# Performance work log

Measured on AMD Instinct MI355X. Metric: run time of the kernel, lower is better.

The kernel has to match this reference:

```python
import jax, jax.numpy as jnp
import numpy as np

B, CIN, H, W = 16, 128, 56, 56
COUT, KH, KW = 256, 3, 3
STRIDE = (1, 1)
PAD = ((1, 1), (1, 1))


def setup_inputs() -> dict:
    key = jax.random.key(0)
    k1, k2, k3 = jax.random.split(key, 3)
    x = jax.random.normal(k1, (B, CIN, H, W), dtype=jnp.float32)
    weight = jax.random.normal(k2, (COUT, CIN, KH, KW), dtype=jnp.float32) * 0.05
    bias = jax.random.normal(k3, (COUT,), dtype=jnp.float32)
    return {"x": x, "weight": weight, "bias": bias}


def reference(x, weight, bias):
    # Conv2d with zero padding, stride 1 -- identical math to the torch
    # unfold+expand+multiply+triple-sum path.
    dn = jax.lax.conv_dimension_numbers(x.shape, weight.shape, ("NCHW", "OIHW", "NCHW"))
    out = jax.lax.conv_general_dilated(x, weight, STRIDE, PAD, dimension_numbers=dn)
    out = out + bias[None, :, None, None]

    # Sparsity of the elementwise product patches * weight.
    # count_nonzero(x_patch * w) over all (b,hw,ww,co,ci,kh,kw) factorizes as
    # sum over windows of conv(1[x!=0], 1[w!=0]) -- same count without
    # materializing the [B,Hw,Ww,Co,Ci,kh,kw] tensor the torch code builds.
    co, ci, kh, kw = weight.shape
    hw, ww = out.shape[2], out.shape[3]
    num_elements = x.shape[0] * hw * ww * co * ci * kh * kw
    nz_map = jax.lax.conv_general_dilated(
        (x != 0).astype(jnp.float32),
        (weight != 0).astype(jnp.float32),
        STRIDE, PAD, dimension_numbers=dn)
    num_nonzero = jnp.sum(nz_map)
    layer_sparsity = (jnp.float32(num_elements) - num_nonzero) / jnp.float32(num_elements)
    return out, layer_sparsity
```

## Files before the change

### kernel.cpp

```cpp
#include <hip/hip_runtime.h>
#include <hip/hip_bf16.h>

typedef __attribute__((ext_vector_type(8))) short bf16x8;
typedef __attribute__((ext_vector_type(8))) unsigned short ushort8;
typedef __attribute__((ext_vector_type(4))) unsigned short ushort4v;
typedef __attribute__((ext_vector_type(4))) float f32x4;
typedef __attribute__((ext_vector_type(4))) unsigned int uint4v;

#define CIN_  128
#define BATCH 16
#define SP_   3136
#define CO_   256
#define NTOT  50176

#define XP_BYTES   13778944
#define WT_BYTES   589824
#define WS_NEEDED  14447104

__device__ __forceinline__ unsigned short f2bf(float f) {
    unsigned int u = __float_as_uint(f);
    u = (u + 0x7fffu + ((u >> 16) & 1u)) >> 16;
    return (unsigned short)u;
}

__device__ __forceinline__ void gl_lds16(const unsigned short* g, unsigned short* l) {
    __builtin_amdgcn_global_load_lds(
        (const __attribute__((address_space(1))) unsigned int*)g,
        (__attribute__((address_space(3))) unsigned int*)l, 16, 0, 0);
}

__global__ __launch_bounds__(256) void k_aux(
    const float* __restrict__ x, const float* __restrict__ w,
    unsigned short* __restrict__ Wt, unsigned short* __restrict__ xp,
    float* __restrict__ Wcnt, float* __restrict__ part)
{
    __shared__ float T[64][65];
    __shared__ float red9[4][9];
    const int blk = blockIdx.x;
    const int tid = threadIdx.x;

    if (blk < 288) {
        int base = (blk * 256 + tid) * 4;
        float4 v = *(const float4*)(w + base);
        #pragma unroll
        for (int j = 0; j < 4; ++j) {
            int e = base + j;
            int co = e / 1152;
            int r  = e - co * 1152;
            int ci = r / 9;
            int koff = r - ci * 9;
            Wt[(koff * 256 + co) * 128 + ci] = f2bf(((const float*)&v)[j]);
        }
    } else if (blk < 576) {
        int lane = tid & 63;
        int j = (blk - 288) * 4 + (tid >> 6);
        float c = 0.f;
        for (int co = lane; co < 256; co += 64)
            c += (w[(size_t)co * 1152 + j] != 0.0f) ? 1.f : 0.f;
        #pragma unroll
        for (int s = 32; s > 0; s >>= 1) c += __shfl_down(c, s, 64);
        if (lane == 0) Wcnt[j] = c;
    } else if (blk < 2624) {
        int bc = blk - 576;
        int ci = bc & 127;
        int b  = bc >> 7;
        const float* xpk = x + (size_t)bc * SP_;
        float cnt[9];
        #pragma unroll
        for (int k = 0; k < 9; ++k) cnt[k] = 0.f;
        for (int e = tid; e < SP_; e += 256) {
            float v = xpk[e];
            if (v != 0.f) {
                int h = e / 56, w_ = e - h * 56;
                float r0 = (h <= 54) ? 1.f : 0.f;
                float r2 = (h >= 1) ? 1.f : 0.f;
                float c0 = (w_ <= 54) ? 1.f : 0.f;
                float c2 = (w_ >= 1) ? 1.f : 0.f;
                cnt[0] += r0 * c0; cnt[1] += r0; cnt[2] += r0 * c2;
                cnt[3] += c0;      cnt[4] += 1.f; cnt[5] += c2;
                cnt[6] += r2 * c0; cnt[7] += r2; cnt[8] += r2 * c2;
            }
        }
        #pragma unroll
        for (int k = 0; k < 9; ++k) {
            #pragma unroll
            for (int s = 32; s > 0; s >>= 1) cnt[k] += __shfl_down(cnt[k], s, 64);
        }
        if ((tid & 63) == 0) {
            #pragma unroll
            for (int k = 0; k < 9; ++k) red9[tid >> 6][k] = cnt[k];
        }
        __syncthreads();
        if (tid < 9) {
            float s = red9[0][tid] + red9[1][tid] + red9[2][tid] + red9[3][tid];
            part[(ci * 9 + tid) * 16 + b] = s;
        }
    } else if (blk < 4192) {
        int i = blk - 2624;
        int sp0 = (i % 49) * 64;
        int rest = i / 49;
        int ci0 = (rest & 1) * 64;
        int b = rest >> 1;
        const float* xb = x + ((size_t)(b * 128 + ci0)) * SP_ + sp0;
        #pragma unroll
        for (int r = 0; r < 16; ++r) {
            const int ci_l = (tid >> 6) * 16 + r;
            const int sp_l = tid & 63;
            T[sp_l][ci_l] = xb[(size_t)ci_l * SP_ + sp_l];
        }
        __syncthreads();
        #pragma unroll
        for (int r = 0; r < 4; ++r) {
            const int sp_l = (tid >> 4) * 4 + r;
            const int cc   = (tid & 15) * 4;
            const int sp = sp0 + sp_l;
            const int oh = sp / 56, ow = sp - oh * 56;
            ushort4v v;
            #pragma unroll
            for (int j = 0; j < 4; ++j) v[j] = f2bf(T[sp_l][cc + j]);
            *(ushort4v*)&xp[(((size_t)b * 58 + oh + 1) * 58 + (ow + 1)) * 128 + ci0 + cc] = v;
        }
    } else {
        int b = blk - 4192;
        if (tid < 228) {
            int oh, ow;
            if (tid < 58)       { oh = 0;            ow = tid; }
            else if (tid < 116) { oh = 57;           ow = tid - 58; }
            else if (tid < 172) { oh = tid - 116 + 1; ow = 0; }
            else                { oh = tid - 172 + 1; ow = 57; }
            unsigned short* p = xp + (((size_t)b * 58 + oh) * 58 + ow) * 128;
            ushort8 z = {};
            #pragma unroll
            for (int j = 0; j < 16; ++j) *(ushort8*)(p + j * 8) = z;
        }
    }
}

__global__ void k_spars(const float* __restrict__ Wcnt, const float* __restrict__ part,
                        float* __restrict__ out_scalar) {
    __shared__ double red[256];
    int t = threadIdx.x;
    double s = 0.0;
    for (int j = t; j < 1152; j += 256) {
        const float4* p4 = (const float4*)(part + (size_t)j * 16);
        float4 a = p4[0], b = p4[1], c = p4[2], d = p4[3];
        float xs = (a.x + a.y + a.z + a.w) + (b.x + b.y + b.z + b.w)
                 + (c.x + c.y + c.z + c.w) + (d.x + d.y + d.z + d.w);
        s += (double)Wcnt[j] * (double)xs;
    }
    red[t] = s; __syncthreads();
    for (int k = 128; k > 0; k >>= 1) {
        if (t < k) red[t] += red[t + k];
        __syncthreads();
    }
    if (t == 0) {
        const double ne = 14797504512.0;
        out_scalar[0] = (float)((ne - red[0]) / ne);
    }
}

__global__ __launch_bounds__(512, 2) void k_conv8(
    const unsigned short* __restrict__ xp, const unsigned short* __restrict__ Wt,
    const float* __restrict__ bias, float* __restrict__ out)
{
    __shared__ __attribute__((aligned(16))) unsigned short Albs[4 * 8192];
    __shared__ __attribute__((aligned(16))) unsigned short Blbs[4 * 8192];

    const int tid  = threadIdx.x;
    const int lane = tid & 63;
    const int l15  = lane & 15;
    const int w    = tid >> 6;
    const int wm   = w >> 2;
    const int wn   = w & 3;
    const int n0   = blockIdx.x * 256;

    int xoffA[2], woffB[2];
    #pragma unroll
    for (int j = 0; j < 2; ++j) {
        int g   = j * 512 + tid;
        int row = g >> 2;
        int c   = (g & 3) ^ ((row >> 1) & 3);
        int n   = n0 + row;
        int b   = n / SP_;
        int sp  = n - b * SP_;
        int oh  = sp / 56, ow = sp - oh * 56;
        xoffA[j] = ((b * 58 + oh + 1) * 58 + (ow + 1)) * 128 + c * 8;
        woffB[j] = row * 128 + c * 8;
    }

    auto stageA = [&](int slotoff, int xsh) {
        #pragma unroll
        for (int j = 0; j < 2; ++j)
            gl_lds16(xp + xsh + xoffA[j], &Albs[slotoff + (j * 512 + tid) * 8]);
    };
    auto stageB = [&](int slotoff, int wsh) {
        #pragma unroll
        for (int j = 0; j < 2; ++j)
            gl_lds16(Wt + wsh + woffB[j], &Blbs[slotoff + (j * 512 + tid) * 8]);
    };

    f32x4 acc[8][4] = {};
    const int cl = lane >> 4;

#define LDA_(SLOT, R) \
    (*(const bf16x8*)&Albs[(SLOT) * 8192 + ((R) + l15) * 32 + \
        ((cl ^ ((((R) + l15) >> 1) & 3)) * 8)])
#define LDB_(SLOT, R) \
    (*(const bf16x8*)&Blbs[(SLOT) * 8192 + ((R) + l15) * 32 + \
        ((cl ^ ((((R) + l15) >> 1) & 3)) * 8)])

    {
        const int xsh0 = (-59) * 128;
        stageA(0, xsh0);          stageB(0, 0);
        stageA(8192, xsh0 + 32);  stageB(8192, 32);
        asm volatile("s_waitcnt vmcnt(4)" ::: "memory");
        __builtin_amdgcn_s_barrier();
    }

    #pragma unroll 1
    for (int koff = 0; koff < 9; ++koff) {
        #pragma unroll
        for (int q = 0; q < 4; ++q) {
            const int p = koff * 4 + q;
            const int slot = q;

            bf16x8 b_[4], a_[8];
            #pragma unroll
            for (int nn = 0; nn < 4; ++nn) b_[nn] = LDB_(slot, wn * 64 + nn * 16);
            #pragma unroll
            for (int m = 0; m < 8; ++m)    a_[m] = LDA_(slot, wm * 128 + m * 16);

            if (p + 2 <= 35) {
                const int p2  = p + 2;
                const int ko2 = p2 >> 2;
                const int q2  = p2 & 3;
                const int kd2 = ko2 / 3;
                const int xsh = ((kd2 - 1) * 58 + (ko2 - kd2 * 3 - 1)) * 128 + q2 * 32;
                const int wsh = ko2 * 32768 + q2 * 32;
                stageA(q2 * 8192, xsh);
                stageB(q2 * 8192, wsh);
                asm volatile("s_waitcnt vmcnt(4)" ::: "memory");
            } else {
                asm volatile("s_waitcnt vmcnt(0)" ::: "memory");
            }
            __builtin_amdgcn_s_barrier();

            __builtin_amdgcn_s_setprio(1);
            #pragma unroll
            for (int m = 0; m < 8; ++m)
                #pragma unroll
                for (int nn = 0; nn < 4; ++nn)
                    acc[m][nn] = __builtin_amdgcn_mfma_f32_16x16x32_bf16(
                        a_[m], b_[nn], acc[m][nn], 0, 0, 0);
            __builtin_amdgcn_s_setprio(0);
        }
    }

#undef LDA_
#undef LDB_

    #pragma unroll
    for (int m = 0; m < 8; ++m) {
        int n  = n0 + wm * 128 + m * 16 + (lane >> 4) * 4;
        int b  = n / SP_;
        int sp = n - b * SP_;
        #pragma unroll
        for (int nn = 0; nn < 4; ++nn) {
            int co = wn * 64 + nn * 16 + l15;
            f32x4 v = acc[m][nn] + bias[co];
            *(f32x4*)&out[((size_t)(b * CO_ + co)) * SP_ + sp] = v;
        }
    }
}

__global__ void k_wt(const float* __restrict__ w, unsigned short* __restrict__ Wt) {
    int e = blockIdx.x * 256 + threadIdx.x;
    float v = w[e];
    int co = e / 1152;
    int r  = e - co * 1152;
    int ci = r / 9;
    int koff = r - ci * 9;
    Wt[(koff * 256 + co) * 128 + ci] = f2bf(v);
}

__global__ void k_wcnt(const float* __restrict__ w, float* __restrict__ Wcnt) {
    int j = blockIdx.x;
    int lane = threadIdx.x;
    float c = 0.f;
    for (int co = lane; co < 256; co += 64)
        c += (w[(size_t)co * 1152 + j] != 0.0f) ? 1.f : 0.f;
    #pragma unroll
    for (int s = 32; s > 0; s >>= 1) c += __shfl_down(c, s, 64);
    if (lane == 0) Wcnt[j] = c;
}

__global__ void k_xcnt(const float* __restrict__ x, float* __restrict__ Xcnt) {
    int blk = blockIdx.x;
    int ci = blk & 127;
    const float* xpk = x + (size_t)blk * SP_;
    int tid = threadIdx.x;
    float cnt[9];
    #pragma unroll
    for (int k = 0; k < 9; ++k) cnt[k] = 0.f;
    for (int e = tid; e < SP_; e += 256) {
        float v = xpk[e];
        if (v != 0.f) {
            int h = e / 56, w_ = e - h * 56;
            float r0 = (h <= 54) ? 1.f : 0.f;
            float r2 = (h >= 1) ? 1.f : 0.f;
            float c0 = (w_ <= 54) ? 1.f : 0.f;
            float c2 = (w_ >= 1) ? 1.f : 0.f;
            cnt[0] += r0 * c0; cnt[1] += r0; cnt[2] += r0 * c2;
            cnt[3] += c0;      cnt[4] += 1.f; cnt[5] += c2;
            cnt[6] += r2 * c0; cnt[7] += r2; cnt[8] += r2 * c2;
        }
    }
    #pragma unroll
    for (int k = 0; k < 9; ++k) {
        #pragma unroll
        for (int s = 32; s > 0; s >>= 1) cnt[k] += __shfl_down(cnt[k], s, 64);
    }
    if ((tid & 63) == 0) {
        #pragma unroll
        for (int k = 0; k < 9; ++k)
            atomicAdd(&Xcnt[ci * 9 + k], cnt[k]);
    }
}

__global__ void k_spars_f(const float* __restrict__ Wcnt, const float* __restrict__ Xcnt,
                          float* __restrict__ out_scalar) {
    __shared__ double red[256];
    int t = threadIdx.x;
    double s = 0.0;
    for (int j = t; j < 1152; j += 256)
        s += (double)Wcnt[j] * (double)Xcnt[j];
    red[t] = s; __syncthreads();
    for (int k = 128; k > 0; k >>= 1) {
        if (t < k) red[t] += red[t + k];
        __syncthreads();
    }
    if (t == 0) {
        const double ne = 14797504512.0;
        out_scalar[0] = (float)((ne - red[0]) / ne);
    }
}

__global__ __launch_bounds__(256) void k_conv(
    const float* __restrict__ x, const unsigned short* __restrict__ Wt,
    const float* __restrict__ bias, float* __restrict__ out)
{
    __shared__ __attribute__((aligned(16))) unsigned short AldsF[64][40];
    __shared__ __attribute__((aligned(16))) unsigned short BldsF[64][40];

    const int tid  = threadIdx.x;
    const int lane = tid & 63;
    const int wid  = tid >> 6;
    const int wm   = wid >> 1, wn = wid & 1;

    const int n0  = blockIdx.x * 64;
    const int b   = blockIdx.x / 49;
    const int sp0 = n0 - b * SP_;
    const int co0 = blockIdx.y * 64;

    const int a_co = tid >> 2;
    const int a_ci = (tid & 3) * 8;
    const int b_n  = tid & 63;
    const int b_k0 = (tid >> 6) * 8;

    const int sp = sp0 + b_n;
    const int oh = sp / 56, ow = sp - oh * 56;

    f32x4 acc[2][2] = {};
    const float* xb_base = x + (size_t)b * CIN_ * SP_;

    for (int koff = 0; koff < 9; ++koff) {
        const int dh = koff / 3 - 1, dw = koff - (koff / 3) * 3 - 1;
        const int ih = oh + dh, iw = ow + dw;
        const bool valid = ((unsigned)ih < 56u) && ((unsigned)iw < 56u);
        const float* xb = xb_base + sp + dh * 56 + dw;
        const unsigned short* wp = Wt + ((size_t)(koff * 256 + co0 + a_co)) * 128 + a_ci;

        for (int ci0 = 0; ci0 < 128; ci0 += 32) {
            uint4v av = *(const uint4v*)(wp + ci0);
            *(uint4v*)&AldsF[a_co][a_ci] = av;
            ushort8 bv;
            #pragma unroll
            for (int j = 0; j < 8; ++j) {
                int ci = ci0 + b_k0 + j;
                float v = 0.f;
                if (valid) v = xb[(size_t)ci * SP_];
                bv[j] = f2bf(v);
            }
            *(ushort8*)&BldsF[b_n][b_k0] = bv;
            __syncthreads();

            const int row = lane & 15;
            const int kq  = (lane >> 4) * 8;
            bf16x8 a0 = *(const bf16x8*)&AldsF[wm * 32 + row][kq];
            bf16x8 a1 = *(const bf16x8*)&AldsF[wm * 32 + 16 + row][kq];
            bf16x8 bb0 = *(const bf16x8*)&BldsF[wn * 32 + row][kq];
            bf16x8 bb1 = *(const bf16x8*)&BldsF[wn * 32 + 16 + row][kq];
            acc[0][0] = __builtin_amdgcn_mfma_f32_16x16x32_bf16(a0, bb0, acc[0][0], 0, 0, 0);
            acc[0][1] = __builtin_amdgcn_mfma_f32_16x16x32_bf16(a0, bb1, acc[0][1], 0, 0, 0);
            acc[1][0] = __builtin_amdgcn_mfma_f32_16x16x32_bf16(a1, bb0, acc[1][0], 0, 0, 0);
            acc[1][1] = __builtin_amdgcn_mfma_f32_16x16x32_bf16(a1, bb1, acc[1][1], 0, 0, 0);
            __syncthreads();
        }
    }

    const int col = lane & 15;
    const int rb  = (lane >> 4) * 4;
    #pragma unroll
    for (int f = 0; f < 2; ++f) {
        #pragma unroll
        for (int g = 0; g < 2; ++g) {
            int spc = sp0 + wn * 32 + g * 16 + col;
            #pragma unroll
            for (int r = 0; r < 4; ++r) {
                int co = co0 + wm * 32 + f * 16 + rb + r;
                out[((size_t)(b * CO_ + co)) * SP_ + spc] = acc[f][g][r] + bias[co];
            }
        }
    }
}

extern "C" void kernel_launch(void* const* d_in, const int* in_sizes, int n_in,
                              void* d_out, int out_size, void* d_ws, size_t ws_size,
                              hipStream_t stream) {
    const float* x    = (const float*)d_in[0];
    const float* w    = (const float*)d_in[1];
    const float* bias = (const float*)d_in[2];
    float* out = (float*)d_out;

    if (ws_size >= (size_t)WS_NEEDED) {
        unsigned short* xp = (unsigned short*)d_ws;
        unsigned short* Wt = (unsigned short*)((char*)d_ws + XP_BYTES);
        float* Wcnt = (float*)((char*)d_ws + XP_BYTES + WT_BYTES);
        float* part = Wcnt + 1152;

        hipLaunchKernelGGL(k_aux,   dim3(4208),   dim3(256), 0, stream,
                           x, w, Wt, xp, Wcnt, part);
        hipLaunchKernelGGL(k_conv8, dim3(196),    dim3(512), 0, stream, xp, Wt, bias, out);
        hipLaunchKernelGGL(k_spars, dim3(1),      dim3(256), 0, stream, Wcnt, part,
                           out + 12845056);
    } else {
        unsigned short* Wt = (unsigned short*)d_ws;
        float* Wcnt = (float*)((char*)d_ws + WT_BYTES);
        float* Xcnt = Wcnt + 1152;

        hipMemsetAsync((void*)Xcnt, 0, 1152 * sizeof(float), stream);
        hipLaunchKernelGGL(k_wt,      dim3(1152),    dim3(256), 0, stream, w, Wt);
        hipLaunchKernelGGL(k_wcnt,    dim3(1152),    dim3(64),  0, stream, w, Wcnt);
        hipLaunchKernelGGL(k_xcnt,    dim3(2048),    dim3(256), 0, stream, x, Xcnt);
        hipLaunchKernelGGL(k_conv,    dim3(784, 4),  dim3(256), 0, stream, x, Wt, bias, out);
        hipLaunchKernelGGL(k_spars_f, dim3(1),       dim3(256), 0, stream, Wcnt, Xcnt,
                           out + 12845056);
    }
}
```

Measured before the change: 64.61 us.

## Deepen LDS pipeline to three stages with register double-buffered fragments

Restructures the conv implicit-GEMM main loop from a two-ahead global-to-LDS prefetch into a three-stage prefetch over four LDS slots. A/B fragments are double-buffered in registers so the LDS reads for the next k-step are issued before the MFMAs of the current step. The goal is to hide LDS read latency and global load latency behind matrix-core work. The cost is roughly twice the fragment registers, which may reduce occupancy or cause spills, and a hand-unrolled prologue and epilogue with tighter slot reuse.

```diff
diff --git a/kernel.cpp b/kernel.cpp
--- a/kernel.cpp
+++ b/kernel.cpp
@@ -188,15 +188,17 @@
         woffB[j] = row * 128 + c * 8;
     }
 
-    auto stageA = [&](int slotoff, int xsh) {
+    auto stage_p = [&](int p) {
+        int ko = p >> 2, q = p & 3;
+        int kd = ko / 3;
+        int xsh = ((kd - 1) * 58 + (ko - kd * 3 - 1)) * 128 + q * 32;
+        int wsh = ko * 32768 + q * 32;
         #pragma unroll
         for (int j = 0; j < 2; ++j)
-            gl_lds16(xp + xsh + xoffA[j], &Albs[slotoff + (j * 512 + tid) * 8]);
-    };
-    auto stageB = [&](int slotoff, int wsh) {
+            gl_lds16(xp + xsh + xoffA[j], &Albs[q * 8192 + (j * 512 + tid) * 8]);
         #pragma unroll
         for (int j = 0; j < 2; ++j)
-            gl_lds16(Wt + wsh + woffB[j], &Blbs[slotoff + (j * 512 + tid) * 8]);
+            gl_lds16(Wt + wsh + woffB[j], &Blbs[q * 8192 + (j * 512 + tid) * 8]);
     };
 
     f32x4 acc[8][4] = {};
@@ -209,53 +211,64 @@
     (*(const bf16x8*)&Blbs[(SLOT) * 8192 + ((R) + l15) * 32 + \
         ((cl ^ ((((R) + l15) >> 1) & 3)) * 8)])
 
-    {
-        const int xsh0 = (-59) * 128;
-        stageA(0, xsh0);          stageB(0, 0);
-        stageA(8192, xsh0 + 32);  stageB(8192, 32);
+#define RD_(SLOT, A, B)                                                        \
+    {                                                                          \
+        _Pragma("unroll")                                                      \
+        for (int nn = 0; nn < 4; ++nn) B[nn] = LDB_(SLOT, wn * 64 + nn * 16);  \
+        _Pragma("unroll")                                                      \
+        for (int m = 0; m < 8; ++m)    A[m] = LDA_(SLOT, wm * 128 + m * 16);   \
+    }
+
+#define MF_(A, B)                                                              \
+    {                                                                          \
+        __builtin_amdgcn_s_setprio(1);                                         \
+        _Pragma("unroll")                                                      \
+        for (int m = 0; m < 8; ++m)                                            \
+            _Pragma("unroll")                                                  \
+            for (int nn = 0; nn < 4; ++nn)                                     \
+                acc[m][nn] = __builtin_amdgcn_mfma_f32_16x16x32_bf16(          \
+                    A[m], B[nn], acc[m][nn], 0, 0, 0);                         \
+        __builtin_amdgcn_s_setprio(0);                                         \
+    }
+
+    bf16x8 a0[8], b0[4], a1[8], b1[4];
+
+    stage_p(0); stage_p(1); stage_p(2);
+    asm volatile("s_waitcnt vmcnt(8)" ::: "memory");
+    __builtin_amdgcn_s_barrier();
+    RD_(0, a0, b0);
+
+    #pragma unroll 1
+    for (int p = 0; p < 32; p += 2) {
         asm volatile("s_waitcnt vmcnt(4)" ::: "memory");
         __builtin_amdgcn_s_barrier();
-    }
-
-    #pragma unroll 1
-    for (int koff = 0; koff < 9; ++koff) {
-        #pragma unroll
-        for (int q = 0; q < 4; ++q) {
-            const int p = koff * 4 + q;
-            const int slot = q;
-
-            bf16x8 b_[4], a_[8];
-            #pragma unroll
-            for (int nn = 0; nn < 4; ++nn) b_[nn] = LDB_(slot, wn * 64 + nn * 16);
-            #pragma unroll
-            for (int m = 0; m < 8; ++m)    a_[m] = LDA_(slot, wm * 128 + m * 16);
-
-            if (p + 2 <= 35) {
-                const int p2  = p + 2;
-                const int ko2 = p2 >> 2;
-                const int q2  = p2 & 3;
-                const int kd2 = ko2 / 3;
-                const int xsh = ((kd2 - 1) * 58 + (ko2 - kd2 * 3 - 1)) * 128 + q2 * 32;
-                const int wsh = ko2 * 32768 + q2 * 32;
-                stageA(q2 * 8192, xsh);
-                stageB(q2 * 8192, wsh);
-                asm volatile("s_waitcnt vmcnt(4)" ::: "memory");
-            } else {
-                asm volatile("s_waitcnt vmcnt(0)" ::: "memory");
-            }
-            __builtin_amdgcn_s_barrier();
-
-            __builtin_amdgcn_s_setprio(1);
-            #pragma unroll
-            for (int m = 0; m < 8; ++m)
-                #pragma unroll
-                for (int nn = 0; nn < 4; ++nn)
-                    acc[m][nn] = __builtin_amdgcn_mfma_f32_16x16x32_bf16(
-                        a_[m], b_[nn], acc[m][nn], 0, 0, 0);
-            __builtin_amdgcn_s_setprio(0);
-        }
-    }
-
+        stage_p(p + 3);
+        RD_((p + 1) & 3, a1, b1);
+        MF_(a0, b0);
+
+        asm volatile("s_waitcnt vmcnt(4)" ::: "memory");
+        __builtin_amdgcn_s_barrier();
+        stage_p(p + 4);
+        RD_((p + 2) & 3, a0, b0);
+        MF_(a1, b1);
+    }
+    asm volatile("s_waitcnt vmcnt(4)" ::: "memory");
+    __builtin_amdgcn_s_barrier();
+    stage_p(35);
+    RD_(1, a1, b1);
+    MF_(a0, b0);
+    asm volatile("s_waitcnt vmcnt(4)" ::: "memory");
+    __builtin_amdgcn_s_barrier();
+    RD_(2, a0, b0);
+    MF_(a1, b1);
+    asm volatile("s_waitcnt vmcnt(0)" ::: "memory");
+    __builtin_amdgcn_s_barrier();
+    RD_(3, a1, b1);
+    MF_(a0, b0);
+    MF_(a1, b1);
+
+#undef RD_
+#undef MF_
 #undef LDA_
 #undef LDB_
 
```

Result: slower. 73.00 us (+13.0%).

## Shrink conv tile to 128x128 with 784 blocks and XCD-aware block remap

Applied to the files above, without the earlier changes.

Replaces the 256x256-tile, 512-thread implicit-GEMM conv kernel (196 blocks) with a 128x128-tile, 256-thread kernel launched as 784 blocks. Each block now covers half the output channels, and a block-index remap groups neighbouring tiles onto the same XCD. The main loop is flattened, and the LDS reads now come after the barrier instead of overlapping the next stage's issue. This aims to fill all 256 CUs better than 196 blocks could and to improve L2 locality, at the cost of lower per-block data reuse and more global traffic.

```diff
diff --git a/kernel.cpp b/kernel.cpp
--- a/kernel.cpp
+++ b/kernel.cpp
@@ -159,25 +159,29 @@
     }
 }
 
-__global__ __launch_bounds__(512, 2) void k_conv8(
+__global__ __launch_bounds__(256, 2) void k_convp(
     const unsigned short* __restrict__ xp, const unsigned short* __restrict__ Wt,
     const float* __restrict__ bias, float* __restrict__ out)
 {
-    __shared__ __attribute__((aligned(16))) unsigned short Albs[4 * 8192];
-    __shared__ __attribute__((aligned(16))) unsigned short Blbs[4 * 8192];
+    __shared__ __attribute__((aligned(16))) unsigned short Albs[4 * 4096];
+    __shared__ __attribute__((aligned(16))) unsigned short Blbs[4 * 4096];
 
     const int tid  = threadIdx.x;
     const int lane = tid & 63;
     const int l15  = lane & 15;
     const int w    = tid >> 6;
-    const int wm   = w >> 2;
-    const int wn   = w & 3;
-    const int n0   = blockIdx.x * 256;
+    const int wm   = w >> 1;
+    const int wn   = w & 1;
+
+    const int flat = blockIdx.x;
+    const int wg   = (flat & 7) * 98 + (flat >> 3);
+    const int n0   = (wg >> 1) * 128;
+    const int co0  = (wg & 1) * 128;
 
     int xoffA[2], woffB[2];
     #pragma unroll
     for (int j = 0; j < 2; ++j) {
-        int g   = j * 512 + tid;
+        int g   = j * 256 + tid;
         int row = g >> 2;
         int c   = (g & 3) ^ ((row >> 1) & 3);
         int n   = n0 + row;
@@ -185,88 +189,77 @@
         int sp  = n - b * SP_;
         int oh  = sp / 56, ow = sp - oh * 56;
         xoffA[j] = ((b * 58 + oh + 1) * 58 + (ow + 1)) * 128 + c * 8;
-        woffB[j] = row * 128 + c * 8;
-    }
-
-    auto stageA = [&](int slotoff, int xsh) {
+        woffB[j] = (co0 + row) * 128 + c * 8;
+    }
+
+    auto stage_p = [&](int p) {
+        int ko = p >> 2, q = p & 3;
+        int kd = ko / 3;
+        int xsh = ((kd - 1) * 58 + (ko - kd * 3 - 1)) * 128 + q * 32;
+        int wsh = ko * 32768 + q * 32;
         #pragma unroll
         for (int j = 0; j < 2; ++j)
-            gl_lds16(xp + xsh + xoffA[j], &Albs[slotoff + (j * 512 + tid) * 8]);
+            gl_lds16(xp + xsh + xoffA[j], &Albs[q * 4096 + (j * 256 + tid) * 8]);
+        #pragma unroll
+        for (int j = 0; j < 2; ++j)
+            gl_lds16(Wt + wsh + woffB[j], &Blbs[q * 4096 + (j * 256 + tid) * 8]);
     };
-    auto stageB = [&](int slotoff, int wsh) {
-        #pragma unroll
-        for (int j = 0; j < 2; ++j)
-            gl_lds16(Wt + wsh + woffB[j], &Blbs[slotoff + (j * 512 + tid) * 8]);
-    };
-
-    f32x4 acc[8][4] = {};
+
+    f32x4 acc[4][4] = {};
     const int cl = lane >> 4;
 
 #define LDA_(SLOT, R) \
-    (*(const bf16x8*)&Albs[(SLOT) * 8192 + ((R) + l15) * 32 + \
+    (*(const bf16x8*)&Albs[(SLOT) * 4096 + ((R) + l15) * 32 + \
         ((cl ^ ((((R) + l15) >> 1) & 3)) * 8)])
 #define LDB_(SLOT, R) \
-    (*(const bf16x8*)&Blbs[(SLOT) * 8192 + ((R) + l15) * 32 + \
+    (*(const bf16x8*)&Blbs[(SLOT) * 4096 + ((R) + l15) * 32 + \
         ((cl ^ ((((R) + l15) >> 1) & 3)) * 8)])
 
-    {
-        const int xsh0 = (-59) * 128;
-        stageA(0, xsh0);          stageB(0, 0);
-        stageA(8192, xsh0 + 32);  stageB(8192, 32);
-        asm volatile("s_waitcnt vmcnt(4)" ::: "memory");
+    stage_p(0); stage_p(1);
+    asm volatile("s_waitcnt vmcnt(4)" ::: "memory");
+    __builtin_amdgcn_s_barrier();
+
+    #pragma unroll 1
+    for (int p = 0; p < 36; ++p) {
+        const int slot = p & 3;
+
+        if (p < 34) {
+            stage_p(p + 2);
+            asm volatile("s_waitcnt vmcnt(4)" ::: "memory");
+        } else if (p == 34) {
+            asm volatile("s_waitcnt vmcnt(4)" ::: "memory");
+        } else {
+            asm volatile("s_waitcnt vmcnt(0)" ::: "memory");
+        }
         __builtin_amdgcn_s_barrier();
-    }
-
-    #pragma unroll 1
-    for (int koff = 0; koff < 9; ++koff) {
-        #pragma unroll
-        for (int q = 0; q < 4; ++q) {
-            const int p = koff * 4 + q;
-            const int slot = q;
-
-            bf16x8 b_[4], a_[8];
-            #pragma unroll
-            for (int nn = 0; nn < 4; ++nn) b_[nn] = LDB_(slot, wn * 64 + nn * 16);
-            #pragma unroll
-            for (int m = 0; m < 8; ++m)    a_[m] = LDA_(slot, wm * 128 + m * 16);
-
-            if (p + 2 <= 35) {
-                const int p2  = p + 2;
-                const int ko2 = p2 >> 2;
-                const int q2  = p2 & 3;
-                const int kd2 = ko2 / 3;
-                const int xsh = ((kd2 - 1) * 58 + (ko2 - kd2 * 3 - 1)) * 128 + q2 * 32;
-                const int wsh = ko2 * 32768 + q2 * 32;
-                stageA(q2 * 8192, xsh);
-                stageB(q2 * 8192, wsh);
-                asm volatile("s_waitcnt vmcnt(4)" ::: "memory");
-            } else {
-                asm volatile("s_waitcnt vmcnt(0)" ::: "memory");
-            }
-            __builtin_amdgcn_s_barrier();
-
-            __builtin_amdgcn_s_setprio(1);
-            #pragma unroll
-            for (int m = 0; m < 8; ++m)
-                #pragma unroll
-                for (int nn = 0; nn < 4; ++nn)
-                    acc[m][nn] = __builtin_amdgcn_mfma_f32_16x16x32_bf16(
-                        a_[m], b_[nn], acc[m][nn], 0, 0, 0);
-            __builtin_amdgcn_s_setprio(0);
-        }
+
+        bf16x8 b_[4], a_[4];
+        #pragma unroll
+        for (int nn = 0; nn < 4; ++nn) b_[nn] = LDB_(slot, wn * 64 + nn * 16);
+        #pragma unroll
+        for (int m = 0; m < 4; ++m)    a_[m] = LDA_(slot, wm * 64 + m * 16);
+
+        __builtin_amdgcn_s_setprio(1);
+        #pragma unroll
+        for (int m = 0; m < 4; ++m)
+            #pragma unroll
+            for (int nn = 0; nn < 4; ++nn)
+                acc[m][nn] = __builtin_amdgcn_mfma_f32_16x16x32_bf16(
+                    a_[m], b_[nn], acc[m][nn], 0, 0, 0);
+        __builtin_amdgcn_s_setprio(0);
     }
 
 #undef LDA_
 #undef LDB_
 
     #pragma unroll
-    for (int m = 0; m < 8; ++m) {
-        int n  = n0 + wm * 128 + m * 16 + (lane >> 4) * 4;
+    for (int m = 0; m < 4; ++m) {
+        int n  = n0 + wm * 64 + m * 16 + (lane >> 4) * 4;
         int b  = n / SP_;
         int sp = n - b * SP_;
         #pragma unroll
         for (int nn = 0; nn < 4; ++nn) {
-            int co = wn * 64 + nn * 16 + l15;
+            int co = co0 + wn * 64 + nn * 16 + l15;
             f32x4 v = acc[m][nn] + bias[co];
             *(f32x4*)&out[((size_t)(b * CO_ + co)) * SP_ + sp] = v;
         }
@@ -440,7 +433,7 @@
 
         hipLaunchKernelGGL(k_aux,   dim3(4208),   dim3(256), 0, stream,
                            x, w, Wt, xp, Wcnt, part);
-        hipLaunchKernelGGL(k_conv8, dim3(196),    dim3(512), 0, stream, xp, Wt, bias, out);
+        hipLaunchKernelGGL(k_convp, dim3(784),    dim3(256), 0, stream, xp, Wt, bias, out);
         hipLaunchKernelGGL(k_spars, dim3(1),      dim3(256), 0, stream, Wcnt, part,
                            out + 12845056);
     } else {
```

Result: slower. 75.24 us (+16.5%).
